# Kernel tuning notes

Measured on AMD Instinct MI355X. Metric: run time of the kernel, lower is better.

The kernel has to match this reference:

```python
import jax, jax.numpy as jnp
import numpy as np

DIM = 512
NUM_HEADS = 8
DIM_HEAD = DIM // NUM_HEADS


def _xavier(key, shape):
    fan_in, fan_out = shape[0], shape[1]
    a = (6.0 / (fan_in + fan_out)) ** 0.5
    return jax.random.uniform(key, shape, jnp.float32, -a, a)


def setup_inputs() -> dict:
    key = jax.random.key(0)
    ks = jax.random.split(key, 8)
    B, N, M = 2, 2048, 2048
    x = jax.random.normal(ks[0], (B, N, DIM), jnp.float32)
    source = jax.random.normal(ks[1], (B, M, DIM), jnp.float32)
    source_mask = jax.random.randint(ks[2], (B, M), 0, 2) > 0
    Wq = _xavier(ks[3], (DIM, DIM)); bq = jnp.zeros((DIM,), jnp.float32)
    Wk = _xavier(ks[4], (DIM, DIM)); bk = jnp.zeros((DIM,), jnp.float32)
    Wv = _xavier(ks[5], (DIM, DIM)); bv = jnp.zeros((DIM,), jnp.float32)
    Wm = _xavier(ks[6], (DIM, DIM)); bm = jnp.zeros((DIM,), jnp.float32)
    return {"x": x, "source": source, "source_mask": source_mask,
            "Wq": Wq, "bq": bq, "Wk": Wk, "bk": bk,
            "Wv": Wv, "bv": bv, "Wm": Wm, "bm": bm}


def reference(x, source, source_mask, Wq, bq, Wk, bk, Wv, bv, Wm, bm):
    B, N, D = x.shape
    M = source.shape[-2]
    H, Dh = NUM_HEADS, DIM_HEAD
    # projections (torch Linear: x @ W^T + b)
    q = (x @ Wq.T + bq).reshape(B, N, H, Dh)
    k = (source @ Wk.T + bk).reshape(B, M, H, Dh)
    v = (source @ Wv.T + bv).reshape(B, M, H, Dh)
    scale = 1.0 / (Dh ** 0.5)
    # scores: [B, N, M, H]
    scores = jnp.einsum('bnhd,bmhd->bnmh', q, k) * scale
    scores = jnp.where(source_mask[:, None, :, None], scores, -jnp.inf)
    prob = jax.nn.softmax(scores, axis=-2)  # softmax over m
    agg = jnp.einsum('bnmh,bmhd->bnhd', prob, v).reshape(B, N, D)
    return agg @ Wm.T + bm
```

## Files before the change

kernel.cpp:

```cpp
#include <hip/hip_runtime.h>
#include <hip/hip_bf16.h>

#define DIMF 512
#define NHEAD 8
#define DHEAD 64
#define BATCH 2
#define SEQN 2048
#define SEQM 2048
#define FPS 40
#define QSCALE 0.18033688011112042f

typedef unsigned short u16;
typedef __attribute__((ext_vector_type(8))) short bf16x8;
typedef __attribute__((ext_vector_type(4))) float f32x4;

static __device__ __forceinline__ u16 f2bf(float f) {
    unsigned u = __float_as_uint(f);
    u += 0x7FFF + ((u >> 16) & 1);
    return (u16)(u >> 16);
}
static __device__ __forceinline__ u16 f2bf_fast(float f) {
    return (u16)((__float_as_uint(f) + 0x8000u) >> 16);
}

static __device__ __forceinline__
void load16(const u16* g, u16* l) {
    __builtin_amdgcn_global_load_lds(
        (const __attribute__((address_space(1))) void*)g,
        (__attribute__((address_space(3))) void*)l,
        16, 0, 0);
}

__global__ __launch_bounds__(256)
void cvt_w(const float* __restrict__ wq, const float* __restrict__ wk,
           const float* __restrict__ wv, const float* __restrict__ wm,
           const int* __restrict__ mask,
           u16* __restrict__ wqb, u16* __restrict__ wkb,
           u16* __restrict__ wvb, u16* __restrict__ wmb,
           u16* __restrict__ maskbf)
{
    int i = (blockIdx.x * 256 + threadIdx.x) * 4;
    if (blockIdx.y == 4) {
        if (i < BATCH * SEQM) {
            int4 m4 = *(const int4*)&mask[i];
            *(ushort4*)&maskbf[i] = make_ushort4(m4.x ? 0x3F80 : 0, m4.y ? 0x3F80 : 0,
                                                 m4.z ? 0x3F80 : 0, m4.w ? 0x3F80 : 0);
        }
        return;
    }
    const float* in = (blockIdx.y == 0) ? wq : (blockIdx.y == 1) ? wk
                    : (blockIdx.y == 2) ? wv : wm;
    u16* out = (blockIdx.y == 0) ? wqb : (blockIdx.y == 1) ? wkb
             : (blockIdx.y == 2) ? wvb : wmb;
    if (i >= DIMF * DIMF) return;
    float4 v = *(const float4*)&in[i];
    *(ushort4*)&out[i] = make_ushort4(f2bf(v.x), f2bf(v.y), f2bf(v.z), f2bf(v.w));
}

__device__ __forceinline__
void gemm_mfma(const float* __restrict__ Xf, const u16* __restrict__ Xb,
               const u16* __restrict__ W, const float* __restrict__ bias,
               const int* __restrict__ msk, void* __restrict__ Out, int mode)
{
    __shared__ u16 As[64 * FPS];
    __shared__ u16 Bs[128 * FPS];

    const int tid  = threadIdx.x;
    const int wave = tid >> 6;
    const int lane = tid & 63;
    const int l15  = lane & 15;
    const int quad = lane >> 4;
    const int wm = wave & 1, wn = wave >> 1;
    const int r0 = blockIdx.x * 64, c0 = blockIdx.y * 128;

    f32x4 acc[2][4] = {};

    const int br = tid >> 2, boct = tid & 3;
    const int ar = tid >> 3, aseg = tid & 7;

    for (int k0 = 0; k0 < DIMF; k0 += 32) {
        bf16x8 bv0 = *(const bf16x8*)&W[(size_t)(c0 + br) * DIMF + k0 + boct * 8];
        bf16x8 bv1 = *(const bf16x8*)&W[(size_t)(c0 + br + 64) * DIMF + k0 + boct * 8];
        float4 a0, a1; bf16x8 av;
        if (Xf) {
            a0 = *(const float4*)&Xf[(size_t)(r0 + ar) * DIMF + k0 + aseg * 4];
            a1 = *(const float4*)&Xf[(size_t)(r0 + ar + 32) * DIMF + k0 + aseg * 4];
        } else {
            av = *(const bf16x8*)&Xb[(size_t)(r0 + br) * DIMF + k0 + boct * 8];
        }
        __syncthreads();
        if (Xf) {
            *(ushort4*)&As[ar * FPS + aseg * 4] =
                make_ushort4(f2bf(a0.x), f2bf(a0.y), f2bf(a0.z), f2bf(a0.w));
            *(ushort4*)&As[(ar + 32) * FPS + aseg * 4] =
                make_ushort4(f2bf(a1.x), f2bf(a1.y), f2bf(a1.z), f2bf(a1.w));
        } else {
            *(bf16x8*)&As[br * FPS + boct * 8] = av;
        }
        *(bf16x8*)&Bs[br * FPS + boct * 8] = bv0;
        *(bf16x8*)&Bs[(br + 64) * FPS + boct * 8] = bv1;
        __syncthreads();

        bf16x8 af[2], bf[4];
        #pragma unroll
        for (int mi = 0; mi < 2; ++mi)
            af[mi] = *(const bf16x8*)&As[(wm * 32 + mi * 16 + l15) * FPS + quad * 8];
        #pragma unroll
        for (int ni = 0; ni < 4; ++ni)
            bf[ni] = *(const bf16x8*)&Bs[(wn * 64 + ni * 16 + l15) * FPS + quad * 8];
        #pragma unroll
        for (int mi = 0; mi < 2; ++mi)
            #pragma unroll
            for (int ni = 0; ni < 4; ++ni)
                acc[mi][ni] = __builtin_amdgcn_mfma_f32_16x16x32_bf16(
                    af[mi], bf[ni], acc[mi][ni], 0, 0, 0);
    }

    float bb[4];
    #pragma unroll
    for (int ni = 0; ni < 4; ++ni)
        bb[ni] = bias[c0 + wn * 64 + ni * 16 + l15];

    #pragma unroll
    for (int mi = 0; mi < 2; ++mi) {
        const int Rbase = r0 + wm * 32 + mi * 16 + quad * 4;
        const int b = Rbase >> 11;
        const int nb = Rbase & (SEQN - 1);
        float mm[4] = {1.f, 1.f, 1.f, 1.f};
        if (mode == 2) {
            int4 m4 = *(const int4*)&msk[b * SEQM + nb];
            mm[0] = m4.x ? 1.f : 0.f; mm[1] = m4.y ? 1.f : 0.f;
            mm[2] = m4.z ? 1.f : 0.f; mm[3] = m4.w ? 1.f : 0.f;
        }
        #pragma unroll
        for (int ni = 0; ni < 4; ++ni) {
            const int C = c0 + wn * 64 + ni * 16 + l15;
            const int h = C >> 6, d = C & 63;
            if (mode == 0) {
                u16* ow = (u16*)Out;
                #pragma unroll
                for (int r = 0; r < 4; ++r)
                    ow[(((size_t)(b * NHEAD + h) * SEQN) + nb + r) * DHEAD + d] =
                        f2bf((acc[mi][ni][r] + bb[ni]) * QSCALE);
            } else if (mode == 1) {
                u16* ow = (u16*)Out;
                #pragma unroll
                for (int r = 0; r < 4; ++r)
                    ow[(((size_t)(b * NHEAD + h) * SEQN) + nb + r) * DHEAD + d] =
                        f2bf(acc[mi][ni][r] + bb[ni]);
            } else if (mode == 2) {
                u16* ow = (u16*)Out;
                #pragma unroll
                for (int r = 0; r < 4; ++r)
                    ow[(((size_t)(b * NHEAD + h) * SEQN) + nb + r) * DHEAD + d] =
                        f2bf((acc[mi][ni][r] + bb[ni]) * mm[r]);
            } else {
                float* ow = (float*)Out;
                #pragma unroll
                for (int r = 0; r < 4; ++r)
                    ow[(size_t)(Rbase + r) * DIMF + C] = acc[mi][ni][r] + bb[ni];
            }
        }
    }
}

__global__ __launch_bounds__(256, 4)
void qkv_proj(const float* __restrict__ x, const float* __restrict__ src,
              const u16* __restrict__ wqb, const float* __restrict__ bq,
              const u16* __restrict__ wkb, const float* __restrict__ bk,
              const u16* __restrict__ wvb, const float* __restrict__ bv,
              const int* __restrict__ mask,
              u16* __restrict__ qw, u16* __restrict__ kw, u16* __restrict__ vw)
{
    const int z = blockIdx.z;
    const float* X = (z == 0) ? x : src;
    const u16* W = (z == 0) ? wqb : (z == 1) ? wkb : wvb;
    const float* B = (z == 0) ? bq : (z == 1) ? bk : bv;
    void* O = (z == 0) ? (void*)qw : (z == 1) ? (void*)kw : (void*)vw;
    gemm_mfma(X, nullptr, W, B, mask, O, z);
}

__global__ __launch_bounds__(256, 4)
void out_proj(const u16* __restrict__ aggb, const u16* __restrict__ wmb,
              const float* __restrict__ bm, float* __restrict__ out)
{
    gemm_mfma(nullptr, aggb, wmb, bm, nullptr, (void*)out, 3);
}

__global__ __launch_bounds__(256)
void vtr(const u16* __restrict__ v, u16* __restrict__ vt)
{
    __shared__ u16 T[64 * 72];
    const int tid = threadIdx.x;
    const int m0 = blockIdx.x * 64, bh = blockIdx.y;
    const u16* src = v + ((size_t)bh * SEQM + m0) * DHEAD;
    const int r = tid >> 3, c = (tid & 7) << 3;
    *(bf16x8*)&T[r * 72 + c]        = *(const bf16x8*)&src[r * DHEAD + c];
    *(bf16x8*)&T[(r + 32) * 72 + c] = *(const bf16x8*)&src[(r + 32) * DHEAD + c];
    __syncthreads();
    const int d = tid >> 2, mc = (tid & 3) << 4;
    u16 tmp[16];
    #pragma unroll
    for (int j = 0; j < 16; ++j) tmp[j] = T[(mc + j) * 72 + d];
    u16* dst = vt + ((size_t)bh * DHEAD + d) * SEQM + m0 + mc;
    *(bf16x8*)&dst[0] = *(bf16x8*)&tmp[0];
    *(bf16x8*)&dst[8] = *(bf16x8*)&tmp[8];
}

__global__ __launch_bounds__(256, 4)
void flash_attn_mfma(const u16* __restrict__ q, const u16* __restrict__ k,
                     const u16* __restrict__ vt, const u16* __restrict__ maskbf,
                     u16* __restrict__ agg)
{
    __shared__ __align__(16) u16 Ks[4096];
    __shared__ __align__(16) u16 Vts[4096];
    __shared__ u16 Ps[4][16 * FPS];
    float* Osum = (float*)Ks;
    float* Lsum = (float*)Vts;

    const int tid  = threadIdx.x;
    const int wave = tid >> 6;
    const int lane = tid & 63;
    const int l15  = lane & 15;
    const int quad = lane >> 4;
    const int qg = wave >> 1, mh = wave & 1;
    const int qt = blockIdx.x, h = blockIdx.y, b = blockIdx.z;
    const int n0 = qt * 32;
    const size_t hoff = (size_t)(b * NHEAD + h) * (size_t)SEQM * DHEAD;
    const u16* kb = k  + hoff;
    const u16* vb = vt + hoff;
    const u16* mb = maskbf + b * SEQM;

    const int dr   = lane >> 3;
    const int doct = (lane & 7) ^ (dr & 7);
    const int g0 = wave, g1 = 4 + wave;
    const u16* kq0 = kb + (size_t)(g0 * 8 + dr) * DHEAD + doct * 8;
    const u16* kq1 = kb + (size_t)(g1 * 8 + dr) * DHEAD + doct * 8;
    const u16* vq0 = vb + (size_t)(g0 * 8 + dr) * SEQM + doct * 8;
    const u16* vq1 = vb + (size_t)(g1 * 8 + dr) * SEQM + doct * 8;
    u16* kl0 = Ks  + g0 * 512;  u16* kl1 = Ks  + g1 * 512;
    u16* vl0 = Vts + g0 * 512;  u16* vl1 = Vts + g1 * 512;

    bf16x8 qf[2];
    {
        const u16* qp = q + hoff + (size_t)(n0 + qg * 16 + l15) * DHEAD + quad * 8;
        qf[0] = *(const bf16x8*)qp;
        qf[1] = *(const bf16x8*)(qp + 32);
    }

    f32x4 O[4] = {};
    f32x4 lacc = {};
    u16* Pw = &Ps[wave][0];
    const int xoct = l15 & 7;

    for (int m0 = 0; m0 < SEQM; m0 += 64) {
        __syncthreads();
        load16(kq0 + (size_t)m0 * DHEAD, kl0);
        load16(kq1 + (size_t)m0 * DHEAD, kl1);
        load16(vq0 + m0, vl0);
        load16(vq1 + m0, vl1);
        __syncthreads();

        f32x4 st[2] = {};
        #pragma unroll
        for (int sub = 0; sub < 2; ++sub) {
            const int mrow = 32 * mh + 16 * sub + l15;
            #pragma unroll
            for (int c = 0; c < 2; ++c) {
                const int oct = (4 * c + quad) ^ xoct;
                bf16x8 af = *(const bf16x8*)&Ks[mrow * 64 + oct * 8];
                st[sub] = __builtin_amdgcn_mfma_f32_16x16x32_bf16(af, qf[c], st[sub], 0, 0, 0);
            }
        }

        #pragma unroll
        for (int sub = 0; sub < 2; ++sub) {
            ushort4 w4 = make_ushort4(
                f2bf_fast(__builtin_amdgcn_exp2f(st[sub][0])),
                f2bf_fast(__builtin_amdgcn_exp2f(st[sub][1])),
                f2bf_fast(__builtin_amdgcn_exp2f(st[sub][2])),
                f2bf_fast(__builtin_amdgcn_exp2f(st[sub][3])));
            *(ushort4*)&Pw[l15 * FPS + 16 * sub + 4 * quad] = w4;
        }

        bf16x8 pf = *(const bf16x8*)&Pw[l15 * FPS + quad * 8];
        bf16x8 mf = *(const bf16x8*)&mb[m0 + 32 * mh + quad * 8];
        lacc = __builtin_amdgcn_mfma_f32_16x16x32_bf16(pf, mf, lacc, 0, 0, 0);
        #pragma unroll
        for (int sd = 0; sd < 4; ++sd) {
            const int d = 16 * sd + l15;
            const int oct = (4 * mh + quad) ^ xoct;
            bf16x8 vf = *(const bf16x8*)&Vts[d * 64 + oct * 8];
            O[sd] = __builtin_amdgcn_mfma_f32_16x16x32_bf16(pf, vf, O[sd], 0, 0, 0);
        }
    }

    __syncthreads();
    if (mh == 1) {
        #pragma unroll
        for (int sd = 0; sd < 4; ++sd)
            #pragma unroll
            for (int r = 0; r < 4; ++r)
                Osum[qg * 1024 + (quad * 4 + r) * 64 + 16 * sd + l15] = O[sd][r];
        if (l15 == 0) {
            #pragma unroll
            for (int r = 0; r < 4; ++r) Lsum[qg * 16 + quad * 4 + r] = lacc[r];
        }
    }
    __syncthreads();
    if (mh == 0) {
        #pragma unroll
        for (int r = 0; r < 4; ++r) {
            const float inv = 1.f / (lacc[r] + Lsum[qg * 16 + quad * 4 + r]);
            const int n = n0 + qg * 16 + quad * 4 + r;
            u16* ag = agg + ((size_t)b * SEQN + n) * DIMF + h * DHEAD + l15;
            #pragma unroll
            for (int sd = 0; sd < 4; ++sd)
                ag[16 * sd] = f2bf((O[sd][r] +
                    Osum[qg * 1024 + (quad * 4 + r) * 64 + 16 * sd + l15]) * inv);
        }
    }
}

extern "C" void kernel_launch(void* const* d_in, const int* in_sizes, int n_in,
                              void* d_out, int out_size, void* d_ws, size_t ws_size,
                              hipStream_t stream)
{
    (void)in_sizes; (void)n_in; (void)out_size; (void)ws_size;
    const float* x      = (const float*)d_in[0];
    const float* source = (const float*)d_in[1];
    const int*   mask   = (const int*)  d_in[2];
    const float* Wq = (const float*)d_in[3]; const float* bq = (const float*)d_in[4];
    const float* Wk = (const float*)d_in[5]; const float* bk = (const float*)d_in[6];
    const float* Wv = (const float*)d_in[7]; const float* bv = (const float*)d_in[8];
    const float* Wm = (const float*)d_in[9]; const float* bm = (const float*)d_in[10];
    float* out = (float*)d_out;

    const size_t SZ = (size_t)BATCH * SEQN * DIMF;
    const size_t WZ = (size_t)DIMF * DIMF;
    u16* qw   = (u16*)d_ws;
    u16* kw   = qw  + SZ;
    u16* vw   = kw  + SZ;
    u16* aggb = vw;
    u16* vtw  = vw  + SZ;
    u16* wqb  = vtw + SZ;
    u16* wkb  = wqb + WZ;
    u16* wvb  = wkb + WZ;
    u16* wmb  = wvb + WZ;
    u16* maskbf = wmb + WZ;

    dim3 gcvt((WZ / 4 + 255) / 256, 5);
    cvt_w<<<gcvt, 256, 0, stream>>>(Wq, Wk, Wv, Wm, mask,
                                    wqb, wkb, wvb, wmb, maskbf);

    dim3 gproj(4096 / 64, 512 / 128, 3);
    qkv_proj<<<gproj, 256, 0, stream>>>(x, source, wqb, bq, wkb, bk, wvb, bv,
                                        mask, qw, kw, vw);

    dim3 gvtr(SEQM / 64, BATCH * NHEAD);
    vtr<<<gvtr, 256, 0, stream>>>(vw, vtw);

    dim3 gattn(SEQN / 32, NHEAD, BATCH);
    flash_attn_mfma<<<gattn, 256, 0, stream>>>(qw, kw, vtw, maskbf, aggb);

    dim3 gout(4096 / 64, 512 / 128);
    out_proj<<<gout, 256, 0, stream>>>(aggb, wmb, bm, out);
}
```

Baseline: 153.0 us.

## Fuse V transpose into projection epilogue and double query rows per attention block

Result: no change. 154.3 us (+0.8%).

```diff
diff --git a/kernel.cpp b/kernel.cpp
--- a/kernel.cpp
+++ b/kernel.cpp
@@ -62,8 +62,9 @@
                const u16* __restrict__ W, const float* __restrict__ bias,
                const int* __restrict__ msk, void* __restrict__ Out, int mode)
 {
-    __shared__ u16 As[64 * FPS];
-    __shared__ u16 Bs[128 * FPS];
+    __shared__ __align__(16) u16 SH[7680];
+    u16* As = SH;
+    u16* Bs = SH + 64 * FPS;
 
     const int tid  = threadIdx.x;
     const int wave = tid >> 6;
@@ -121,17 +122,48 @@
     for (int ni = 0; ni < 4; ++ni)
         bb[ni] = bias[c0 + wn * 64 + ni * 16 + l15];
 
+    if (mode == 2) {
+        u16* T = SH;
+        const int b = r0 >> 11;
+        const int n_base = r0 & (SEQN - 1);
+        #pragma unroll
+        for (int hh = 0; hh < 2; ++hh) {
+            __syncthreads();
+            if (wn == hh) {
+                #pragma unroll
+                for (int mi = 0; mi < 2; ++mi) {
+                    const int rl = wm * 32 + mi * 16 + quad * 4;
+                    int4 m4 = *(const int4*)&msk[b * SEQM + n_base + rl];
+                    float mm[4];
+                    mm[0] = m4.x ? 1.f : 0.f; mm[1] = m4.y ? 1.f : 0.f;
+                    mm[2] = m4.z ? 1.f : 0.f; mm[3] = m4.w ? 1.f : 0.f;
+                    #pragma unroll
+                    for (int ni = 0; ni < 4; ++ni)
+                        #pragma unroll
+                        for (int r = 0; r < 4; ++r)
+                            T[(rl + r) * 72 + ni * 16 + l15] =
+                                f2bf((acc[mi][ni][r] + bb[ni]) * mm[r]);
+                }
+            }
+            __syncthreads();
+            const int d = tid >> 2, ms = (tid & 3) << 4;
+            u16 tmp[16];
+            #pragma unroll
+            for (int j = 0; j < 16; ++j) tmp[j] = T[(ms + j) * 72 + d];
+            const int hgl = (c0 >> 6) + hh;
+            u16* dst = (u16*)Out + ((size_t)(b * NHEAD + hgl) * DHEAD + d) * SEQM
+                       + n_base + ms;
+            *(bf16x8*)&dst[0] = *(bf16x8*)&tmp[0];
+            *(bf16x8*)&dst[8] = *(bf16x8*)&tmp[8];
+        }
+        return;
+    }
+
     #pragma unroll
     for (int mi = 0; mi < 2; ++mi) {
         const int Rbase = r0 + wm * 32 + mi * 16 + quad * 4;
         const int b = Rbase >> 11;
         const int nb = Rbase & (SEQN - 1);
-        float mm[4] = {1.f, 1.f, 1.f, 1.f};
-        if (mode == 2) {
-            int4 m4 = *(const int4*)&msk[b * SEQM + nb];
-            mm[0] = m4.x ? 1.f : 0.f; mm[1] = m4.y ? 1.f : 0.f;
-            mm[2] = m4.z ? 1.f : 0.f; mm[3] = m4.w ? 1.f : 0.f;
-        }
         #pragma unroll
         for (int ni = 0; ni < 4; ++ni) {
             const int C = c0 + wn * 64 + ni * 16 + l15;
@@ -148,12 +180,6 @@
                 for (int r = 0; r < 4; ++r)
                     ow[(((size_t)(b * NHEAD + h) * SEQN) + nb + r) * DHEAD + d] =
                         f2bf(acc[mi][ni][r] + bb[ni]);
-            } else if (mode == 2) {
-                u16* ow = (u16*)Out;
-                #pragma unroll
-                for (int r = 0; r < 4; ++r)
-                    ow[(((size_t)(b * NHEAD + h) * SEQN) + nb + r) * DHEAD + d] =
-                        f2bf((acc[mi][ni][r] + bb[ni]) * mm[r]);
             } else {
                 float* ow = (float*)Out;
                 #pragma unroll
@@ -170,13 +196,13 @@
               const u16* __restrict__ wkb, const float* __restrict__ bk,
               const u16* __restrict__ wvb, const float* __restrict__ bv,
               const int* __restrict__ mask,
-              u16* __restrict__ qw, u16* __restrict__ kw, u16* __restrict__ vw)
+              u16* __restrict__ qw, u16* __restrict__ kw, u16* __restrict__ vtw)
 {
     const int z = blockIdx.z;
     const float* X = (z == 0) ? x : src;
     const u16* W = (z == 0) ? wqb : (z == 1) ? wkb : wvb;
     const float* B = (z == 0) ? bq : (z == 1) ? bk : bv;
-    void* O = (z == 0) ? (void*)qw : (z == 1) ? (void*)kw : (void*)vw;
+    void* O = (z == 0) ? (void*)qw : (z == 1) ? (void*)kw : (void*)vtw;
     gemm_mfma(X, nullptr, W, B, mask, O, z);
 }
 
@@ -187,36 +213,17 @@
     gemm_mfma(nullptr, aggb, wmb, bm, nullptr, (void*)out, 3);
 }
 
-__global__ __launch_bounds__(256)
-void vtr(const u16* __restrict__ v, u16* __restrict__ vt)
-{
-    __shared__ u16 T[64 * 72];
-    const int tid = threadIdx.x;
-    const int m0 = blockIdx.x * 64, bh = blockIdx.y;
-    const u16* src = v + ((size_t)bh * SEQM + m0) * DHEAD;
-    const int r = tid >> 3, c = (tid & 7) << 3;
-    *(bf16x8*)&T[r * 72 + c]        = *(const bf16x8*)&src[r * DHEAD + c];
-    *(bf16x8*)&T[(r + 32) * 72 + c] = *(const bf16x8*)&src[(r + 32) * DHEAD + c];
-    __syncthreads();
-    const int d = tid >> 2, mc = (tid & 3) << 4;
-    u16 tmp[16];
-    #pragma unroll
-    for (int j = 0; j < 16; ++j) tmp[j] = T[(mc + j) * 72 + d];
-    u16* dst = vt + ((size_t)bh * DHEAD + d) * SEQM + m0 + mc;
-    *(bf16x8*)&dst[0] = *(bf16x8*)&tmp[0];
-    *(bf16x8*)&dst[8] = *(bf16x8*)&tmp[8];
-}
-
-__global__ __launch_bounds__(256, 4)
+__global__ __launch_bounds__(256, 2)
 void flash_attn_mfma(const u16* __restrict__ q, const u16* __restrict__ k,
                      const u16* __restrict__ vt, const u16* __restrict__ maskbf,
                      u16* __restrict__ agg)
 {
-    __shared__ __align__(16) u16 Ks[4096];
-    __shared__ __align__(16) u16 Vts[4096];
-    __shared__ u16 Ps[4][16 * FPS];
-    float* Osum = (float*)Ks;
-    float* Lsum = (float*)Vts;
+    __shared__ __align__(16) u16 SH[13312];
+    u16* Ks  = SH;
+    u16* Vts = SH + 4096;
+    u16* Ps  = SH + 8192;
+    float* Osum = (float*)SH;
+    float* Lsum = (float*)(SH + 8192);
 
     const int tid  = threadIdx.x;
     const int wave = tid >> 6;
@@ -224,8 +231,8 @@
     const int l15  = lane & 15;
     const int quad = lane >> 4;
     const int qg = wave >> 1, mh = wave & 1;
-    const int qt = blockIdx.x, h = blockIdx.y, b = blockIdx.z;
-    const int n0 = qt * 32;
+    const int h = blockIdx.y, b = blockIdx.z;
+    const int n0 = blockIdx.x * 64;
     const size_t hoff = (size_t)(b * NHEAD + h) * (size_t)SEQM * DHEAD;
     const u16* kb = k  + hoff;
     const u16* vb = vt + hoff;
@@ -241,16 +248,18 @@
     u16* kl0 = Ks  + g0 * 512;  u16* kl1 = Ks  + g1 * 512;
     u16* vl0 = Vts + g0 * 512;  u16* vl1 = Vts + g1 * 512;
 
-    bf16x8 qf[2];
-    {
-        const u16* qp = q + hoff + (size_t)(n0 + qg * 16 + l15) * DHEAD + quad * 8;
-        qf[0] = *(const bf16x8*)qp;
-        qf[1] = *(const bf16x8*)(qp + 32);
-    }
-
-    f32x4 O[4] = {};
-    f32x4 lacc = {};
-    u16* Pw = &Ps[wave][0];
+    bf16x8 qf[2][2];
+    #pragma unroll
+    for (int qh = 0; qh < 2; ++qh) {
+        const u16* qp = q + hoff + (size_t)(n0 + qg * 32 + qh * 16 + l15) * DHEAD
+                        + quad * 8;
+        qf[qh][0] = *(const bf16x8*)qp;
+        qf[qh][1] = *(const bf16x8*)(qp + 32);
+    }
+
+    f32x4 O[2][4] = {};
+    f32x4 lacc[2] = {};
+    u16* Pw = Ps + wave * (32 * FPS);
     const int xoct = l15 & 7;
 
     for (int m0 = 0; m0 < SEQM; m0 += 64) {
@@ -261,7 +270,7 @@
         load16(vq1 + m0, vl1);
         __syncthreads();
 
-        f32x4 st[2] = {};
+        f32x4 st[2][2] = {};
         #pragma unroll
         for (int sub = 0; sub < 2; ++sub) {
             const int mrow = 32 * mh + 16 * sub + l15;
@@ -269,56 +278,77 @@
             for (int c = 0; c < 2; ++c) {
                 const int oct = (4 * c + quad) ^ xoct;
                 bf16x8 af = *(const bf16x8*)&Ks[mrow * 64 + oct * 8];
-                st[sub] = __builtin_amdgcn_mfma_f32_16x16x32_bf16(af, qf[c], st[sub], 0, 0, 0);
-            }
-        }
-
-        #pragma unroll
-        for (int sub = 0; sub < 2; ++sub) {
-            ushort4 w4 = make_ushort4(
-                f2bf_fast(__builtin_amdgcn_exp2f(st[sub][0])),
-                f2bf_fast(__builtin_amdgcn_exp2f(st[sub][1])),
-                f2bf_fast(__builtin_amdgcn_exp2f(st[sub][2])),
-                f2bf_fast(__builtin_amdgcn_exp2f(st[sub][3])));
-            *(ushort4*)&Pw[l15 * FPS + 16 * sub + 4 * quad] = w4;
-        }
-
-        bf16x8 pf = *(const bf16x8*)&Pw[l15 * FPS + quad * 8];
+                #pragma unroll
+                for (int qh = 0; qh < 2; ++qh)
+                    st[qh][sub] = __builtin_amdgcn_mfma_f32_16x16x32_bf16(
+                        af, qf[qh][c], st[qh][sub], 0, 0, 0);
+            }
+        }
+
+        #pragma unroll
+        for (int qh = 0; qh < 2; ++qh)
+            #pragma unroll
+            for (int sub = 0; sub < 2; ++sub) {
+                ushort4 w4 = make_ushort4(
+                    f2bf_fast(__builtin_amdgcn_exp2f(st[qh][sub][0])),
+                    f2bf_fast(__builtin_amdgcn_exp2f(st[qh][sub][1])),
+                    f2bf_fast(__builtin_amdgcn_exp2f(st[qh][sub][2])),
+                    f2bf_fast(__builtin_amdgcn_exp2f(st[qh][sub][3])));
+                *(ushort4*)&Pw[(qh * 16 + l15) * FPS + 16 * sub + 4 * quad] = w4;
+            }
+
+        bf16x8 vf[4];
+        #pragma unroll
+        for (int sd = 0; sd < 4; ++sd) {
+            const int oct = (4 * mh + quad) ^ xoct;
+            vf[sd] = *(const bf16x8*)&Vts[(16 * sd + l15) * 64 + oct * 8];
+        }
         bf16x8 mf = *(const bf16x8*)&mb[m0 + 32 * mh + quad * 8];
-        lacc = __builtin_amdgcn_mfma_f32_16x16x32_bf16(pf, mf, lacc, 0, 0, 0);
-        #pragma unroll
-        for (int sd = 0; sd < 4; ++sd) {
-            const int d = 16 * sd + l15;
-            const int oct = (4 * mh + quad) ^ xoct;
-            bf16x8 vf = *(const bf16x8*)&Vts[d * 64 + oct * 8];
-            O[sd] = __builtin_amdgcn_mfma_f32_16x16x32_bf16(pf, vf, O[sd], 0, 0, 0);
+
+        #pragma unroll
+        for (int qh = 0; qh < 2; ++qh) {
+            bf16x8 pf = *(const bf16x8*)&Pw[(qh * 16 + l15) * FPS + quad * 8];
+            lacc[qh] = __builtin_amdgcn_mfma_f32_16x16x32_bf16(pf, mf, lacc[qh], 0, 0, 0);
+            #pragma unroll
+            for (int sd = 0; sd < 4; ++sd)
+                O[qh][sd] = __builtin_amdgcn_mfma_f32_16x16x32_bf16(
+                    pf, vf[sd], O[qh][sd], 0, 0, 0);
         }
     }
 
     __syncthreads();
     if (mh == 1) {
         #pragma unroll
-        for (int sd = 0; sd < 4; ++sd)
-            #pragma unroll
-            for (int r = 0; r < 4; ++r)
-                Osum[qg * 1024 + (quad * 4 + r) * 64 + 16 * sd + l15] = O[sd][r];
-        if (l15 == 0) {
-            #pragma unroll
-            for (int r = 0; r < 4; ++r) Lsum[qg * 16 + quad * 4 + r] = lacc[r];
+        for (int qh = 0; qh < 2; ++qh) {
+            #pragma unroll
+            for (int sd = 0; sd < 4; ++sd)
+                #pragma unroll
+                for (int r = 0; r < 4; ++r)
+                    Osum[qg * 2048 + (qh * 16 + quad * 4 + r) * 64 + 16 * sd + l15]
+                        = O[qh][sd][r];
+            if (l15 == 0) {
+                #pragma unroll
+                for (int r = 0; r < 4; ++r)
+                    Lsum[qg * 32 + qh * 16 + quad * 4 + r] = lacc[qh][r];
+            }
         }
     }
     __syncthreads();
     if (mh == 0) {
         #pragma unroll
-        for (int r = 0; r < 4; ++r) {
-            const float inv = 1.f / (lacc[r] + Lsum[qg * 16 + quad * 4 + r]);
-            const int n = n0 + qg * 16 + quad * 4 + r;
-            u16* ag = agg + ((size_t)b * SEQN + n) * DIMF + h * DHEAD + l15;
-            #pragma unroll
-            for (int sd = 0; sd < 4; ++sd)
-                ag[16 * sd] = f2bf((O[sd][r] +
-                    Osum[qg * 1024 + (quad * 4 + r) * 64 + 16 * sd + l15]) * inv);
-        }
+        for (int qh = 0; qh < 2; ++qh)
+            #pragma unroll
+            for (int r = 0; r < 4; ++r) {
+                const float inv = 1.f /
+                    (lacc[qh][r] + Lsum[qg * 32 + qh * 16 + quad * 4 + r]);
+                const int n = n0 + qg * 32 + qh * 16 + quad * 4 + r;
+                u16* ag = agg + ((size_t)b * SEQN + n) * DIMF + h * DHEAD + l15;
+                #pragma unroll
+                for (int sd = 0; sd < 4; ++sd)
+                    ag[16 * sd] = f2bf((O[qh][sd][r] +
+                        Osum[qg * 2048 + (qh * 16 + quad * 4 + r) * 64 + 16 * sd + l15])
+                        * inv);
+            }
     }
 }
 
@@ -340,10 +370,9 @@
     const size_t WZ = (size_t)DIMF * DIMF;
     u16* qw   = (u16*)d_ws;
     u16* kw   = qw  + SZ;
-    u16* vw   = kw  + SZ;
-    u16* aggb = vw;
-    u16* vtw  = vw  + SZ;
-    u16* wqb  = vtw + SZ;
+    u16* vtw  = kw  + SZ;
+    u16* aggb = vtw + SZ;
+    u16* wqb  = aggb + SZ;
     u16* wkb  = wqb + WZ;
     u16* wvb  = wkb + WZ;
     u16* wmb  = wvb + WZ;
@@ -355,12 +384,9 @@
 
     dim3 gproj(4096 / 64, 512 / 128, 3);
     qkv_proj<<<gproj, 256, 0, stream>>>(x, source, wqb, bq, wkb, bk, wvb, bv,
-                                        mask, qw, kw, vw);
-
-    dim3 gvtr(SEQM / 64, BATCH * NHEAD);
-    vtr<<<gvtr, 256, 0, stream>>>(vw, vtw);
-
-    dim3 gattn(SEQN / 32, NHEAD, BATCH);
+                                        mask, qw, kw, vtw);
+
+    dim3 gattn(SEQN / 64, NHEAD, BATCH);
     flash_attn_mfma<<<gattn, 256, 0, stream>>>(qw, kw, vtw, maskbf, aggb);
 
     dim3 gout(4096 / 64, 512 / 128);
```
